# Optimization experiments

Measured on AMD Instinct MI355X. Metric: run time of the kernel, lower is better.

The kernel has to match this reference:

```python
import jax, jax.numpy as jnp
import numpy as np

B, L, D = 4, 2048, 1024
H, KD, VD = 16, 64, 64
EPS = 1e-5


def setup_inputs() -> dict:
    key = jax.random.key(0)
    ks = jax.random.split(key, 12)
    s_in = 1.0 / np.sqrt(D)
    s_out = 1.0 / np.sqrt(H * VD)
    return {
        "queries": jax.random.normal(ks[0], (B, L, D), dtype=jnp.float32),
        "Wq": jax.random.uniform(ks[1], (D, H * KD), jnp.float32, -s_in, s_in),
        "bq": jax.random.uniform(ks[2], (H * KD,), jnp.float32, -s_in, s_in),
        "Wk": jax.random.uniform(ks[3], (D, H * KD), jnp.float32, -s_in, s_in),
        "bk": jax.random.uniform(ks[4], (H * KD,), jnp.float32, -s_in, s_in),
        "Wv": jax.random.uniform(ks[5], (D, H * VD), jnp.float32, -s_in, s_in),
        "bv": jax.random.uniform(ks[6], (H * VD,), jnp.float32, -s_in, s_in),
        "Wo": jax.random.uniform(ks[7], (H * VD, D), jnp.float32, -s_out, s_out),
        "bo": jax.random.uniform(ks[8], (D,), jnp.float32, -s_out, s_out),
        "gamma": jnp.ones((D,), jnp.float32),
        "beta": jnp.zeros((D,), jnp.float32),
    }


def reference(queries, Wq, bq, Wk, bk, Wv, bv, Wo, bo, gamma, beta):
    # QKV projections -> [B, L, H, head_dim]
    q = (queries @ Wq + bq).reshape(B, L, H, KD)
    k = (queries @ Wk + bk).reshape(B, L, H, KD)
    v = (queries @ Wv + bv).reshape(B, L, H, VD)
    # scaled dot-product attention per head: scores [B, H, Lq, Lk]
    scores = jnp.einsum("bqhd,bkhd->bhqk", q, k) / np.sqrt(KD).astype(np.float32)
    attn = jax.nn.softmax(scores, axis=-1)
    out = jnp.einsum("bhqk,bkhd->bqhd", attn, v).reshape(B, L, H * VD)
    # out projection (dropout is identity in eval), residual + LayerNorm
    res = out @ Wo + bo + queries
    mu = jnp.mean(res, axis=-1, keepdims=True)
    var = jnp.var(res, axis=-1, keepdims=True)
    return (res - mu) / jnp.sqrt(var + EPS) * gamma + beta
```

## Files before the change

### kernel.cpp

```cpp
#include <hip/hip_runtime.h>
#include <hip/hip_bf16.h>

#define BATCH 4
#define SEQ   2048
#define DIM   1024
#define NHEAD 16
#define HDIM  64
#define EPS_LN 1e-5f
#define QSCALE 0.18033688011112042f

typedef __attribute__((ext_vector_type(8))) short short8;
typedef __attribute__((ext_vector_type(4))) float f32x4;
typedef __attribute__((ext_vector_type(16))) float f32x16;
typedef __attribute__((ext_vector_type(4))) unsigned uint32x4;

__device__ __forceinline__ unsigned short f2bf(float x) {
    __hip_bfloat16 h = __float2bfloat16(x);
    return *reinterpret_cast<unsigned short*>(&h);
}
__device__ __forceinline__ unsigned int pack2bf(float a, float b) {
    __hip_bfloat162 h = __float22bfloat162_rn(float2{a, b});
    return *reinterpret_cast<unsigned int*>(&h);
}

__device__ __forceinline__ void pl32_swap(unsigned& a, unsigned& b) {
    asm("v_permlane32_swap_b32 %0, %1" : "+v"(a), "+v"(b));
}

__device__ __forceinline__ void gl_lds16(const void* g, void* l) {
    __builtin_amdgcn_global_load_lds(
        (const __attribute__((address_space(1))) unsigned int*)g,
        (__attribute__((address_space(3))) unsigned int*)l,
        16, 0, 0);
}

__global__ __launch_bounds__(256) void prep_kernel(const float* __restrict__ W0,
                                                   const float* __restrict__ W1,
                                                   const float* __restrict__ W2,
                                                   const float* __restrict__ W3,
                                                   const float* __restrict__ queries,
                                                   unsigned short* __restrict__ Wqkvt,
                                                   unsigned short* __restrict__ Wot,
                                                   unsigned short* __restrict__ qout)
{
    const int z = blockIdx.z;
    const int t = threadIdx.x;

    if (z == 4) {
        const int nthr = 16 * 16 * 256;
        int i = (blockIdx.y * 16 + blockIdx.x) * 256 + t;
        for (int it = 0; it < (BATCH * SEQ * DIM / 4) / nthr; it++, i += nthr) {
            float4 v = ((const float4*)queries)[i];
            ushort4 u;
            u.x = f2bf(v.x); u.y = f2bf(v.y); u.z = f2bf(v.z); u.w = f2bf(v.w);
            ((ushort4*)qout)[i] = u;
        }
        return;
    }

    __shared__ float Ts[64][65];
    const float* W = (z == 0) ? W0 : (z == 1) ? W1 : (z == 2) ? W2 : W3;
    unsigned short* Wt = (z == 3) ? Wot : (Wqkvt + (size_t)z * DIM * DIM);

    const int k0 = blockIdx.y * 64, n0 = blockIdx.x * 64;
    const int lr = t >> 2, lq = t & 3;

#pragma unroll
    for (int i = 0; i < 4; i++) {
        float4 v = *(const float4*)(W + (size_t)(k0 + lr) * DIM + n0 + (lq * 4 + i) * 4);
        Ts[lr][(lq * 4 + i) * 4 + 0] = v.x;
        Ts[lr][(lq * 4 + i) * 4 + 1] = v.y;
        Ts[lr][(lq * 4 + i) * 4 + 2] = v.z;
        Ts[lr][(lq * 4 + i) * 4 + 3] = v.w;
    }
    __syncthreads();
#pragma unroll
    for (int i = 0; i < 4; i++) {
        const int c = lq * 16 + i * 4;
        ushort4 u;
        u.x = f2bf(Ts[c + 0][lr]);
        u.y = f2bf(Ts[c + 1][lr]);
        u.z = f2bf(Ts[c + 2][lr]);
        u.w = f2bf(Ts[c + 3][lr]);
        *(ushort4*)(Wt + (size_t)(n0 + lr) * DIM + k0 + c) = u;
    }
}

__global__ __launch_bounds__(256) void gemm_qkv(const unsigned short* __restrict__ A,
                                                const unsigned short* __restrict__ Bt,
                                                const float* __restrict__ bq,
                                                const float* __restrict__ bk,
                                                const float* __restrict__ bv,
                                                unsigned short* __restrict__ Qbf,
                                                unsigned short* __restrict__ Kbf,
                                                unsigned short* __restrict__ Vtb)
{
    __shared__ __attribute__((aligned(16))) unsigned short As[128 * 32];
    __shared__ __attribute__((aligned(16))) unsigned short Bs[128 * 32];

    const int tid = threadIdx.x;
    const int w = tid >> 6, lane = tid & 63;
    const int col = lane & 15, quad = lane >> 4;
    const int wm = (w >> 1) * 64, wn = (w & 1) * 64;
    const int m0 = blockIdx.y * 128, n0 = blockIdx.x * 128;

    f32x4 acc[4][4] = {};
    const int srow = tid >> 2, sc4 = tid & 3;

    for (int k0 = 0; k0 < DIM; k0 += 32) {
        __syncthreads();
#pragma unroll
        for (int it = 0; it < 2; it++) {
            gl_lds16(A  + (size_t)(m0 + srow + it * 64) * DIM + k0 + sc4 * 8,
                     (char*)As + w * 1024 + it * 4096);
            gl_lds16(Bt + (size_t)(n0 + srow + it * 64) * DIM + k0 + sc4 * 8,
                     (char*)Bs + w * 1024 + it * 4096);
        }
        __syncthreads();

        short8 af[4], bf[4];
#pragma unroll
        for (int mt = 0; mt < 4; mt++) af[mt] = *(short8*)&As[(wm + mt * 16 + col) * 32 + quad * 8];
#pragma unroll
        for (int nt = 0; nt < 4; nt++) bf[nt] = *(short8*)&Bs[(wn + nt * 16 + col) * 32 + quad * 8];

#pragma unroll
        for (int mt = 0; mt < 4; mt++)
#pragma unroll
            for (int nt = 0; nt < 4; nt++)
                acc[mt][nt] = __builtin_amdgcn_mfma_f32_16x16x32_bf16(af[mt], bf[nt], acc[mt][nt], 0, 0, 0);
    }

    const int sector = n0 >> 10;
    const float* bias = (sector == 0) ? bq : (sector == 1) ? bk : bv;

#pragma unroll
    for (int nt = 0; nt < 4; nt++) {
        const int n = n0 + wn + nt * 16 + col;
        const int nloc = n - (sector << 10);
        const float bvv = bias[nloc];
#pragma unroll
        for (int mt = 0; mt < 4; mt++) {
            const int mbase = m0 + wm + mt * 16 + quad * 4;
            if (sector == 0) {
#pragma unroll
                for (int r = 0; r < 4; r++)
                    Qbf[(size_t)(mbase + r) * DIM + nloc] = f2bf((acc[mt][nt][r] + bvv) * QSCALE);
            } else if (sector == 1) {
#pragma unroll
                for (int r = 0; r < 4; r++)
                    Kbf[(size_t)(mbase + r) * DIM + nloc] = f2bf(acc[mt][nt][r] + bvv);
            } else {
                const int h = nloc >> 6, d = nloc & 63;
                const int b = mbase >> 11, l = mbase & 2047;
                ushort4 u;
                u.x = f2bf(acc[mt][nt][0] + bvv);
                u.y = f2bf(acc[mt][nt][1] + bvv);
                u.z = f2bf(acc[mt][nt][2] + bvv);
                u.w = f2bf(acc[mt][nt][3] + bvv);
                *(ushort4*)(Vtb + ((size_t)((b * NHEAD + h) * HDIM + d)) * SEQ + l) = u;
            }
        }
    }
}

__global__ __launch_bounds__(256) void gemm_out(const unsigned short* __restrict__ A,
                                                const unsigned short* __restrict__ Bt,
                                                const float* __restrict__ bias,
                                                const float* __restrict__ resid,
                                                float* __restrict__ Cout)
{
    __shared__ __attribute__((aligned(16))) unsigned short As[128 * 32];
    __shared__ __attribute__((aligned(16))) unsigned short Bs[128 * 32];

    const int tid = threadIdx.x;
    const int w = tid >> 6, lane = tid & 63;
    const int col = lane & 15, quad = lane >> 4;
    const int wm = (w >> 1) * 64, wn = (w & 1) * 64;
    const int m0 = blockIdx.y * 128, n0 = blockIdx.x * 128;

    f32x4 acc[4][4] = {};
    const int srow = tid >> 2, sc4 = tid & 3;

    for (int k0 = 0; k0 < DIM; k0 += 32) {
        __syncthreads();
#pragma unroll
        for (int it = 0; it < 2; it++) {
            gl_lds16(A  + (size_t)(m0 + srow + it * 64) * DIM + k0 + sc4 * 8,
                     (char*)As + w * 1024 + it * 4096);
            gl_lds16(Bt + (size_t)(n0 + srow + it * 64) * DIM + k0 + sc4 * 8,
                     (char*)Bs + w * 1024 + it * 4096);
        }
        __syncthreads();

        short8 af[4], bf[4];
#pragma unroll
        for (int mt = 0; mt < 4; mt++) af[mt] = *(short8*)&As[(wm + mt * 16 + col) * 32 + quad * 8];
#pragma unroll
        for (int nt = 0; nt < 4; nt++) bf[nt] = *(short8*)&Bs[(wn + nt * 16 + col) * 32 + quad * 8];

#pragma unroll
        for (int mt = 0; mt < 4; mt++)
#pragma unroll
            for (int nt = 0; nt < 4; nt++)
                acc[mt][nt] = __builtin_amdgcn_mfma_f32_16x16x32_bf16(af[mt], bf[nt], acc[mt][nt], 0, 0, 0);
    }

#pragma unroll
    for (int nt = 0; nt < 4; nt++) {
        const int n = n0 + wn + nt * 16 + col;
        const float bvv = bias[n];
#pragma unroll
        for (int mt = 0; mt < 4; mt++) {
            const int mbase = m0 + wm + mt * 16 + quad * 4;
#pragma unroll
            for (int r = 0; r < 4; r++) {
                const size_t off = (size_t)(mbase + r) * DIM + n;
                Cout[off] = acc[mt][nt][r] + bvv + resid[off];
            }
        }
    }
}

__global__ __launch_bounds__(512) void attn_mfma(const unsigned short* __restrict__ Qb,
                                                 const unsigned short* __restrict__ Kb,
                                                 const unsigned short* __restrict__ Vt,
                                                 unsigned short* __restrict__ Ob)
{
    __shared__ __attribute__((aligned(16))) unsigned short Ks[2 * 64 * 64];
    __shared__ __attribute__((aligned(16))) unsigned short Vs[2 * 64 * 64];
    __shared__ float DsX[128];

    const int tid = threadIdx.x;
    const int w = tid >> 6, lane = tid & 63;
    const int qw = w & 3, kw = w >> 2;
    const int l31 = lane & 31, hi = lane >> 5;
    const int sw7 = l31 & 7;

    const int bh  = blockIdx.x & 63;
    const int qt_ = blockIdx.x >> 6;
    const int b   = bh >> 4;
    const int h   = bh & 15;

    const int q0 = qt_ * 128 + qw * 32;

    short8 qf[4];
#pragma unroll
    for (int ds = 0; ds < 4; ds++)
        qf[ds] = *(const short8*)(Qb + ((size_t)(b * SEQ) + q0 + l31) * DIM + h * HDIM + ds * 16 + hi * 8);

    f32x16 o[2] = {};
    float dsum = 0.f;

    const size_t kbase0 = ((size_t)(b * SEQ)) * DIM + h * HDIM;
    const size_t vbase0 = ((size_t)((b * NHEAD + h) * HDIM)) * SEQ;

    const int lr  = lane >> 3;
    const int swc = (lane & 7) ^ lr;

    {
        const int row = w * 8 + lr;
        gl_lds16(Kb + kbase0 + (size_t)row * DIM + swc * 8, (char*)Ks + w * 1024);
        gl_lds16(Vt + vbase0 + (size_t)row * SEQ + swc * 8, (char*)Vs + w * 1024);
    }
    __syncthreads();

    for (int kt = 0; kt < SEQ / 64; kt++) {
        const int cur = kt & 1, nxt = cur ^ 1;
        const unsigned short* Ksb = Ks + cur * 4096;
        const unsigned short* Vsb = Vs + cur * 4096;

        if (kt + 1 < SEQ / 64) {
            const int row = w * 8 + lr;
            gl_lds16(Kb + kbase0 + (size_t)((kt + 1) * 64 + row) * DIM + swc * 8,
                     (char*)Ks + nxt * 8192 + w * 1024);
            gl_lds16(Vt + vbase0 + (size_t)row * SEQ + (kt + 1) * 64 + swc * 8,
                     (char*)Vs + nxt * 8192 + w * 1024);
        }

        f32x16 s = {};
#pragma unroll
        for (int ds = 0; ds < 4; ds++) {
            short8 kf = *(const short8*)&Ksb[(kw * 32 + l31) * 64 + (((ds * 2 + hi) ^ sw7) * 8)];
            s = __builtin_amdgcn_mfma_f32_32x32x16_bf16(kf, qf[ds], s, 0, 0, 0);
        }
        unsigned d0, d1, d2, d3, d4, d5, d6, d7;
        {
            float p0, p1;
            p0 = __builtin_amdgcn_exp2f(s[0]);  p1 = __builtin_amdgcn_exp2f(s[1]);
            dsum += p0 + p1;  d0 = pack2bf(p0, p1);
            p0 = __builtin_amdgcn_exp2f(s[2]);  p1 = __builtin_amdgcn_exp2f(s[3]);
            dsum += p0 + p1;  d1 = pack2bf(p0, p1);
            p0 = __builtin_amdgcn_exp2f(s[4]);  p1 = __builtin_amdgcn_exp2f(s[5]);
            dsum += p0 + p1;  d2 = pack2bf(p0, p1);
            p0 = __builtin_amdgcn_exp2f(s[6]);  p1 = __builtin_amdgcn_exp2f(s[7]);
            dsum += p0 + p1;  d3 = pack2bf(p0, p1);
            p0 = __builtin_amdgcn_exp2f(s[8]);  p1 = __builtin_amdgcn_exp2f(s[9]);
            dsum += p0 + p1;  d4 = pack2bf(p0, p1);
            p0 = __builtin_amdgcn_exp2f(s[10]); p1 = __builtin_amdgcn_exp2f(s[11]);
            dsum += p0 + p1;  d5 = pack2bf(p0, p1);
            p0 = __builtin_amdgcn_exp2f(s[12]); p1 = __builtin_amdgcn_exp2f(s[13]);
            dsum += p0 + p1;  d6 = pack2bf(p0, p1);
            p0 = __builtin_amdgcn_exp2f(s[14]); p1 = __builtin_amdgcn_exp2f(s[15]);
            dsum += p0 + p1;  d7 = pack2bf(p0, p1);
        }
        pl32_swap(d0, d2);  pl32_swap(d1, d3);
        pl32_swap(d4, d6);  pl32_swap(d5, d7);
        short8 pf0 = __builtin_bit_cast(short8, uint32x4{d0, d1, d2, d3});
        short8 pf1 = __builtin_bit_cast(short8, uint32x4{d4, d5, d6, d7});

        __builtin_amdgcn_s_setprio(1);
#pragma unroll
        for (int db = 0; db < 2; db++) {
            short8 vf0 = *(const short8*)&Vsb[(db * 32 + l31) * 64 + (((kw * 4 + 0 + hi) ^ sw7) * 8)];
            short8 vf1 = *(const short8*)&Vsb[(db * 32 + l31) * 64 + (((kw * 4 + 2 + hi) ^ sw7) * 8)];
            o[db] = __builtin_amdgcn_mfma_f32_32x32x16_bf16(vf0, pf0, o[db], 0, 0, 0);
            o[db] = __builtin_amdgcn_mfma_f32_32x32x16_bf16(vf1, pf1, o[db], 0, 0, 0);
        }
        __builtin_amdgcn_s_setprio(0);

        __syncthreads();
    }

    const float ds_h = dsum + __shfl_xor(dsum, 32);

    if (kw == 1) {
        if (hi == 0) DsX[qw * 32 + l31] = ds_h;
        float* p0 = (float*)Ks + (size_t)(qw * 64 + lane) * 16;
        float* p1 = (float*)Vs + (size_t)(qw * 64 + lane) * 16;
        *(f32x16*)p0 = o[0];
        *(f32x16*)p1 = o[1];
    }
    __syncthreads();
    if (kw == 0) {
        const float den = ds_h + DsX[qw * 32 + l31];
        const float inv = 1.f / den;
        const float* p0 = (const float*)Ks + (size_t)(qw * 64 + lane) * 16;
        const float* p1 = (const float*)Vs + (size_t)(qw * 64 + lane) * 16;
        const f32x16 o0p = *(const f32x16*)p0;
        const f32x16 o1p = *(const f32x16*)p1;
        o[0] += o0p;
        o[1] += o1p;

        const size_t rowoff = ((size_t)(b * SEQ) + q0 + l31) * DIM + h * HDIM;
#pragma unroll
        for (int db = 0; db < 2; db++)
#pragma unroll
            for (int g = 0; g < 4; g++) {
                ushort4 u;
                u.x = f2bf(o[db][g * 4 + 0] * inv);
                u.y = f2bf(o[db][g * 4 + 1] * inv);
                u.z = f2bf(o[db][g * 4 + 2] * inv);
                u.w = f2bf(o[db][g * 4 + 3] * inv);
                *(ushort4*)(Ob + rowoff + db * 32 + g * 8 + hi * 4) = u;
            }
    }
}

__global__ __launch_bounds__(256) void layernorm_kernel(float* __restrict__ res,
                                                        const float* __restrict__ gamma,
                                                        const float* __restrict__ beta)
{
    const int tid = threadIdx.x;
    const int row = blockIdx.x;
    float4 xv = ((const float4*)(res + (size_t)row * DIM))[tid];

    float s  = xv.x + xv.y + xv.z + xv.w;
    float sq = xv.x * xv.x + xv.y * xv.y + xv.z * xv.z + xv.w * xv.w;
#pragma unroll
    for (int off = 32; off; off >>= 1) {
        s  += __shfl_xor(s, off);
        sq += __shfl_xor(sq, off);
    }
    __shared__ float sm[8];
    const int w = tid >> 6, lane = tid & 63;
    if (lane == 0) { sm[w] = s; sm[4 + w] = sq; }
    __syncthreads();
    const float st  = sm[0] + sm[1] + sm[2] + sm[3];
    const float sqt = sm[4] + sm[5] + sm[6] + sm[7];
    const float mu   = st * (1.f / DIM);
    const float var  = sqt * (1.f / DIM) - mu * mu;
    const float rstd = rsqrtf(var + EPS_LN);

    float4 g  = ((const float4*)gamma)[tid];
    float4 be = ((const float4*)beta)[tid];
    float4 o;
    o.x = (xv.x - mu) * rstd * g.x + be.x;
    o.y = (xv.y - mu) * rstd * g.y + be.y;
    o.z = (xv.z - mu) * rstd * g.z + be.z;
    o.w = (xv.w - mu) * rstd * g.w + be.w;
    ((float4*)(res + (size_t)row * DIM))[tid] = o;
}

extern "C" void kernel_launch(void* const* d_in, const int* in_sizes, int n_in,
                              void* d_out, int out_size, void* d_ws, size_t ws_size,
                              hipStream_t stream)
{
    const float* queries = (const float*)d_in[0];
    const float* Wq = (const float*)d_in[1];
    const float* bq = (const float*)d_in[2];
    const float* Wk = (const float*)d_in[3];
    const float* bk = (const float*)d_in[4];
    const float* Wv = (const float*)d_in[5];
    const float* bv = (const float*)d_in[6];
    const float* Wo = (const float*)d_in[7];
    const float* bo = (const float*)d_in[8];
    const float* gamma = (const float*)d_in[9];
    const float* beta  = (const float*)d_in[10];
    float* outp = (float*)d_out;

    const int M = BATCH * SEQ;
    const size_t BUF = (size_t)M * DIM;
    const size_t WSZ = (size_t)DIM * DIM;

    unsigned short* w0  = (unsigned short*)d_ws;
    unsigned short* qin = w0;
    unsigned short* Qbf = w0 + BUF;
    unsigned short* Kbf = w0 + 2 * BUF;
    unsigned short* Vtb = w0 + 3 * BUF;
    unsigned short* Wqkvt = w0 + 4 * BUF;
    unsigned short* Wot   = Wqkvt + 3 * WSZ;
    unsigned short* Obf = qin;

    dim3 blk(256);

    dim3 pgrid(DIM / 64, DIM / 64, 5);
    prep_kernel<<<pgrid, blk, 0, stream>>>(Wq, Wk, Wv, Wo, queries, Wqkvt, Wot, qin);

    dim3 qkvgrid(3 * DIM / 128, M / 128);
    gemm_qkv<<<qkvgrid, blk, 0, stream>>>(qin, Wqkvt, bq, bk, bv, Qbf, Kbf, Vtb);

    attn_mfma<<<BATCH * NHEAD * (SEQ / 128), dim3(512), 0, stream>>>(Qbf, Kbf, Vtb, Obf);

    dim3 ogrid(DIM / 128, M / 128);
    gemm_out<<<ogrid, blk, 0, stream>>>(Obf, Wot, bo, queries, outp);

    layernorm_kernel<<<M, blk, 0, stream>>>(outp, gamma, beta);
}
```

Baseline: 311.6 us.

## Split attention PV work by output head-dim instead of key half

The attention kernel's eight waves were split by query block and key half, with the two key halves reduced through LDS at the end. Now each wave owns a 32-wide slice of the output head dimension and processes all 64 keys per tile, so no cross-wave partial reduction or extra barrier is needed. The cost is that QK^T scores and exp are computed twice, once per output half, which doubles the score MFMA and exp work.

```diff
diff --git a/kernel.cpp b/kernel.cpp
--- a/kernel.cpp
+++ b/kernel.cpp
@@ -229,11 +229,10 @@
 {
     __shared__ __attribute__((aligned(16))) unsigned short Ks[2 * 64 * 64];
     __shared__ __attribute__((aligned(16))) unsigned short Vs[2 * 64 * 64];
-    __shared__ float DsX[128];
 
     const int tid = threadIdx.x;
     const int w = tid >> 6, lane = tid & 63;
-    const int qw = w & 3, kw = w >> 2;
+    const int qw = w & 3, dw = w >> 2;
     const int l31 = lane & 31, hi = lane >> 5;
     const int sw7 = l31 & 7;
 
@@ -249,7 +248,7 @@
     for (int ds = 0; ds < 4; ds++)
         qf[ds] = *(const short8*)(Qb + ((size_t)(b * SEQ) + q0 + l31) * DIM + h * HDIM + ds * 16 + hi * 8);
 
-    f32x16 o[2] = {};
+    f32x16 o = {};
     float dsum = 0.f;
 
     const size_t kbase0 = ((size_t)(b * SEQ)) * DIM + h * HDIM;
@@ -278,82 +277,64 @@
                      (char*)Vs + nxt * 8192 + w * 1024);
         }
 
-        f32x16 s = {};
-#pragma unroll
-        for (int ds = 0; ds < 4; ds++) {
-            short8 kf = *(const short8*)&Ksb[(kw * 32 + l31) * 64 + (((ds * 2 + hi) ^ sw7) * 8)];
-            s = __builtin_amdgcn_mfma_f32_32x32x16_bf16(kf, qf[ds], s, 0, 0, 0);
-        }
-        unsigned d0, d1, d2, d3, d4, d5, d6, d7;
-        {
-            float p0, p1;
-            p0 = __builtin_amdgcn_exp2f(s[0]);  p1 = __builtin_amdgcn_exp2f(s[1]);
-            dsum += p0 + p1;  d0 = pack2bf(p0, p1);
-            p0 = __builtin_amdgcn_exp2f(s[2]);  p1 = __builtin_amdgcn_exp2f(s[3]);
-            dsum += p0 + p1;  d1 = pack2bf(p0, p1);
-            p0 = __builtin_amdgcn_exp2f(s[4]);  p1 = __builtin_amdgcn_exp2f(s[5]);
-            dsum += p0 + p1;  d2 = pack2bf(p0, p1);
-            p0 = __builtin_amdgcn_exp2f(s[6]);  p1 = __builtin_amdgcn_exp2f(s[7]);
-            dsum += p0 + p1;  d3 = pack2bf(p0, p1);
-            p0 = __builtin_amdgcn_exp2f(s[8]);  p1 = __builtin_amdgcn_exp2f(s[9]);
-            dsum += p0 + p1;  d4 = pack2bf(p0, p1);
-            p0 = __builtin_amdgcn_exp2f(s[10]); p1 = __builtin_amdgcn_exp2f(s[11]);
-            dsum += p0 + p1;  d5 = pack2bf(p0, p1);
-            p0 = __builtin_amdgcn_exp2f(s[12]); p1 = __builtin_amdgcn_exp2f(s[13]);
-            dsum += p0 + p1;  d6 = pack2bf(p0, p1);
-            p0 = __builtin_amdgcn_exp2f(s[14]); p1 = __builtin_amdgcn_exp2f(s[15]);
-            dsum += p0 + p1;  d7 = pack2bf(p0, p1);
-        }
-        pl32_swap(d0, d2);  pl32_swap(d1, d3);
-        pl32_swap(d4, d6);  pl32_swap(d5, d7);
-        short8 pf0 = __builtin_bit_cast(short8, uint32x4{d0, d1, d2, d3});
-        short8 pf1 = __builtin_bit_cast(short8, uint32x4{d4, d5, d6, d7});
-
-        __builtin_amdgcn_s_setprio(1);
-#pragma unroll
-        for (int db = 0; db < 2; db++) {
-            short8 vf0 = *(const short8*)&Vsb[(db * 32 + l31) * 64 + (((kw * 4 + 0 + hi) ^ sw7) * 8)];
-            short8 vf1 = *(const short8*)&Vsb[(db * 32 + l31) * 64 + (((kw * 4 + 2 + hi) ^ sw7) * 8)];
-            o[db] = __builtin_amdgcn_mfma_f32_32x32x16_bf16(vf0, pf0, o[db], 0, 0, 0);
-            o[db] = __builtin_amdgcn_mfma_f32_32x32x16_bf16(vf1, pf1, o[db], 0, 0, 0);
-        }
-        __builtin_amdgcn_s_setprio(0);
+#pragma unroll
+        for (int kb = 0; kb < 2; kb++) {
+            f32x16 s = {};
+#pragma unroll
+            for (int ds = 0; ds < 4; ds++) {
+                short8 kf = *(const short8*)&Ksb[(kb * 32 + l31) * 64 + (((ds * 2 + hi) ^ sw7) * 8)];
+                s = __builtin_amdgcn_mfma_f32_32x32x16_bf16(kf, qf[ds], s, 0, 0, 0);
+            }
+            unsigned d0, d1, d2, d3, d4, d5, d6, d7;
+            {
+                float p0, p1;
+                p0 = __builtin_amdgcn_exp2f(s[0]);  p1 = __builtin_amdgcn_exp2f(s[1]);
+                dsum += p0 + p1;  d0 = pack2bf(p0, p1);
+                p0 = __builtin_amdgcn_exp2f(s[2]);  p1 = __builtin_amdgcn_exp2f(s[3]);
+                dsum += p0 + p1;  d1 = pack2bf(p0, p1);
+                p0 = __builtin_amdgcn_exp2f(s[4]);  p1 = __builtin_amdgcn_exp2f(s[5]);
+                dsum += p0 + p1;  d2 = pack2bf(p0, p1);
+                p0 = __builtin_amdgcn_exp2f(s[6]);  p1 = __builtin_amdgcn_exp2f(s[7]);
+                dsum += p0 + p1;  d3 = pack2bf(p0, p1);
+                p0 = __builtin_amdgcn_exp2f(s[8]);  p1 = __builtin_amdgcn_exp2f(s[9]);
+                dsum += p0 + p1;  d4 = pack2bf(p0, p1);
+                p0 = __builtin_amdgcn_exp2f(s[10]); p1 = __builtin_amdgcn_exp2f(s[11]);
+                dsum += p0 + p1;  d5 = pack2bf(p0, p1);
+                p0 = __builtin_amdgcn_exp2f(s[12]); p1 = __builtin_amdgcn_exp2f(s[13]);
+                dsum += p0 + p1;  d6 = pack2bf(p0, p1);
+                p0 = __builtin_amdgcn_exp2f(s[14]); p1 = __builtin_amdgcn_exp2f(s[15]);
+                dsum += p0 + p1;  d7 = pack2bf(p0, p1);
+            }
+            pl32_swap(d0, d2);  pl32_swap(d1, d3);
+            pl32_swap(d4, d6);  pl32_swap(d5, d7);
+            short8 pf0 = __builtin_bit_cast(short8, uint32x4{d0, d1, d2, d3});
+            short8 pf1 = __builtin_bit_cast(short8, uint32x4{d4, d5, d6, d7});
+
+            __builtin_amdgcn_s_setprio(1);
+            {
+                short8 vf0 = *(const short8*)&Vsb[(dw * 32 + l31) * 64 + (((kb * 4 + 0 + hi) ^ sw7) * 8)];
+                short8 vf1 = *(const short8*)&Vsb[(dw * 32 + l31) * 64 + (((kb * 4 + 2 + hi) ^ sw7) * 8)];
+                o = __builtin_amdgcn_mfma_f32_32x32x16_bf16(vf0, pf0, o, 0, 0, 0);
+                o = __builtin_amdgcn_mfma_f32_32x32x16_bf16(vf1, pf1, o, 0, 0, 0);
+            }
+            __builtin_amdgcn_s_setprio(0);
+        }
 
         __syncthreads();
     }
 
-    const float ds_h = dsum + __shfl_xor(dsum, 32);
-
-    if (kw == 1) {
-        if (hi == 0) DsX[qw * 32 + l31] = ds_h;
-        float* p0 = (float*)Ks + (size_t)(qw * 64 + lane) * 16;
-        float* p1 = (float*)Vs + (size_t)(qw * 64 + lane) * 16;
-        *(f32x16*)p0 = o[0];
-        *(f32x16*)p1 = o[1];
-    }
-    __syncthreads();
-    if (kw == 0) {
-        const float den = ds_h + DsX[qw * 32 + l31];
-        const float inv = 1.f / den;
-        const float* p0 = (const float*)Ks + (size_t)(qw * 64 + lane) * 16;
-        const float* p1 = (const float*)Vs + (size_t)(qw * 64 + lane) * 16;
-        const f32x16 o0p = *(const f32x16*)p0;
-        const f32x16 o1p = *(const f32x16*)p1;
-        o[0] += o0p;
-        o[1] += o1p;
-
-        const size_t rowoff = ((size_t)(b * SEQ) + q0 + l31) * DIM + h * HDIM;
-#pragma unroll
-        for (int db = 0; db < 2; db++)
-#pragma unroll
-            for (int g = 0; g < 4; g++) {
-                ushort4 u;
-                u.x = f2bf(o[db][g * 4 + 0] * inv);
-                u.y = f2bf(o[db][g * 4 + 1] * inv);
-                u.z = f2bf(o[db][g * 4 + 2] * inv);
-                u.w = f2bf(o[db][g * 4 + 3] * inv);
-                *(ushort4*)(Ob + rowoff + db * 32 + g * 8 + hi * 4) = u;
-            }
+    const float den = dsum + __shfl_xor(dsum, 32);
+    const float inv = 1.f / den;
+
+    const size_t rowoff = ((size_t)(b * SEQ) + q0 + l31) * DIM + h * HDIM;
+#pragma unroll
+    for (int g = 0; g < 4; g++) {
+        ushort4 u;
+        u.x = f2bf(o[g * 4 + 0] * inv);
+        u.y = f2bf(o[g * 4 + 1] * inv);
+        u.z = f2bf(o[g * 4 + 2] * inv);
+        u.w = f2bf(o[g * 4 + 3] * inv);
+        *(ushort4*)(Ob + rowoff + dw * 32 + g * 8 + hi * 4) = u;
     }
 }
 
```

Result: slower. 361.6 us (+16.0%).
